# Optimization experiments

Measured on AMD Instinct MI355X. Metric: run time of the kernel, lower is better.

The kernel has to match this reference:

```python
import jax, jax.numpy as jnp
import numpy as np

DIM = 128
CODEBOOK_SIZE = 1024

def setup_inputs() -> dict:
    key = jax.random.key(0)
    k1, k2 = jax.random.split(key)
    x = jax.random.normal(k1, (16, 4096, DIM), dtype=jnp.float32)
    embed = jax.random.normal(k2, (CODEBOOK_SIZE, DIM), dtype=jnp.float32)
    return {"x": x, "embed": embed}

def reference(x, embed):
    # preprocess: flatten leading dims -> (N, d)
    shape = x.shape
    flat = x.reshape(-1, shape[-1])  # (N, d)
    x_sq = jnp.sum(flat * flat, axis=1, keepdims=True)        # (N, 1)
    e_sq = jnp.sum(embed * embed, axis=1)[None, :]            # (1, K)
    dist = -(x_sq - 2.0 * (flat @ embed.T) + e_sq)            # (N, K)
    embed_ind = jnp.argmax(dist, axis=-1)                     # (N,)
    embed_ind = embed_ind.reshape(shape[:-1])                 # (...,)
    quantize = jnp.take(embed, embed_ind, axis=0)             # (..., d)
    return (quantize, embed_ind)
```

## Files before the change

### kernel.cpp

```cpp
#include <hip/hip_runtime.h>

#define NRD   65536
#define DIMD  128
#define KCB   1024
#define RPB   64
#define NBLK  (NRD / RPB)
#define MARGIN 0.40f

typedef float f32x4 __attribute__((ext_vector_type(4)));
typedef short short8 __attribute__((ext_vector_type(8)));

#define WS_ESQ   0
#define WS_CNT   4096
#define WS_LIST  8192
#define WS_B     270336
#define WS_ET2   532480
#define WS_NEED  1056768

__device__ inline unsigned short f2bf(float f) {
    unsigned u = __float_as_uint(f);
    u += 0x7FFFu + ((u >> 16) & 1u);
    return (unsigned short)(u >> 16);
}

__device__ inline short8 pack_h(float4 a, float4 b) {
    short8 r;
    r[0]=(short)f2bf(a.x); r[1]=(short)f2bf(a.y); r[2]=(short)f2bf(a.z); r[3]=(short)f2bf(a.w);
    r[4]=(short)f2bf(b.x); r[5]=(short)f2bf(b.y); r[6]=(short)f2bf(b.z); r[7]=(short)f2bf(b.w);
    return r;
}

__global__ __launch_bounds__(256, 2) void prep_kernel(const float* __restrict__ embed,
                                                      float* __restrict__ esq,
                                                      float4* __restrict__ bblob,
                                                      float4* __restrict__ et4,
                                                      int* __restrict__ cnt,
                                                      int doTrans) {
    __shared__ float tile[64][129];
    const int t = threadIdx.x;
    {
        int gw   = blockIdx.x * 4 + (t >> 6);
        int lane = t & 63;
        const float* row = embed + (size_t)gw * DIMD;
        float a = row[lane], b = row[lane + 64];
        float v = a * a + b * b;
        #pragma unroll
        for (int off = 32; off >= 1; off >>= 1) v += __shfl_xor(v, off, 64);
        if (lane == 0) esq[gw] = v;
    }
    if (blockIdx.x < 64) {
        int tid  = blockIdx.x * 256 + t;
        int lane = tid & 63;
        int ctg  = (tid >> 6) & 15;
        int ksh  = (tid >> 10) & 1;
        int s    = tid >> 11;
        int chunk = s >> 1, kh = s & 1;
        int ks = kh * 2 + ksh;
        int l15 = lane & 15, l4 = lane >> 4;
        int code = chunk * 256 + ctg * 16 + l15;
        int d0   = ks * 32 + l4 * 8;
        const float4* e4 = (const float4*)(embed + (size_t)code * DIMD + d0);
        short8 v = pack_h(e4[0], e4[1]);
        bblob[tid] = *(float4*)&v;
    }
    if (doTrans && blockIdx.x >= 64 && blockIdx.x < 80) {
        const int c0 = (blockIdx.x - 64) * 64;
        #pragma unroll
        for (int i = 0; i < 8; ++i) {
            int u = t + i * 256;
            int row = u >> 5, col4 = u & 31;
            float4 v = ((const float4*)embed)[(size_t)(c0 + row) * 32 + col4];
            tile[row][col4 * 4 + 0] = v.x;
            tile[row][col4 * 4 + 1] = v.y;
            tile[row][col4 * 4 + 2] = v.z;
            tile[row][col4 * 4 + 3] = v.w;
        }
        __syncthreads();
        #pragma unroll
        for (int i = 0; i < 8; ++i) {
            int u = t + i * 256;
            int d = u >> 4, off = u & 15;
            float4 v;
            v.x = tile[off * 4 + 0][d];
            v.y = tile[off * 4 + 1][d];
            v.z = tile[off * 4 + 2][d];
            v.w = tile[off * 4 + 3][d];
            et4[(size_t)d * 256 + (c0 >> 2) + off] = v;
        }
    }
    if (blockIdx.x == 128 && t == 0) cnt[0] = 0;
}

__global__ __launch_bounds__(512, 4) void vq_mfma(const float* __restrict__ x,
                                                  const float* __restrict__ embed,
                                                  const float* __restrict__ esq,
                                                  const float4* __restrict__ bblob,
                                                  float* __restrict__ out_q,
                                                  float* __restrict__ out_idx,
                                                  int* __restrict__ cnt,
                                                  int* __restrict__ list) {
    __shared__ __align__(16) short Bb[32][512];
    __shared__ float rbest[4][RPB];
    __shared__ int   rmeta[4][RPB];
    __shared__ float rb2[4][RPB];

    const int t    = threadIdx.x;
    const int lane = t & 63;
    const int w    = __builtin_amdgcn_readfirstlane(t >> 6);
    const int rg   = w >> 2, cg = w & 3;
    const int l15  = lane & 15, l4 = lane >> 4;
    const int row0 = blockIdx.x * RPB;

    short (*Atrans)[4][512] = (short (*)[4][512])&Bb[0][0];

    const int ksA = w & 3, jh = w >> 2;
    const float4* xs = (const float4*)(x + (size_t)(row0 + lane) * DIMD + ksA * 32 + jh * 16);
    float4 xv0 = xs[0], xv1 = xs[1], xv2 = xs[2], xv3 = xs[3];

    const int rtA = lane >> 4, riA = lane & 15;
    *(short8*)&Atrans[ksA][rtA][((jh * 2 + 0) * 16 + riA) * 8] = pack_h(xv0, xv1);
    *(short8*)&Atrans[ksA][rtA][((jh * 2 + 1) * 16 + riA) * 8] = pack_h(xv2, xv3);
    asm volatile("s_waitcnt lgkmcnt(0)" ::: "memory");
    __builtin_amdgcn_s_barrier();

    short8 ahr[4][2];
    #pragma unroll
    for (int ks = 0; ks < 4; ++ks)
        #pragma unroll
        for (int rt = 0; rt < 2; ++rt)
            ahr[ks][rt] = *(const short8*)&Atrans[ks][rg * 2 + rt][lane * 8];
    asm volatile("s_waitcnt lgkmcnt(0)" ::: "memory");
    __builtin_amdgcn_s_barrier();

#define GLDS(sv) do {                                                                                   \
    const char* g_ = (const char*)bblob + (size_t)(sv) * 32768 + ((size_t)w * 64 + lane) * 16;          \
    _Pragma("unroll")                                                                                   \
    for (int k_ = 0; k_ < 4; ++k_)                                                                      \
        __builtin_amdgcn_global_load_lds(                                                               \
            (const __attribute__((address_space(1))) unsigned int*)(g_ + k_ * 8192),                    \
            (__attribute__((address_space(3))) unsigned int*)&Bb[k_ * 8 + w][0], 16, 0, 0);             \
} while (0)

    GLDS(0);
    asm volatile("s_waitcnt vmcnt(0)" ::: "memory");
    __builtin_amdgcn_s_barrier();

    f32x4 acc[2][4];
    float best[2][4]; int bidx[2][4]; float b2[2][4];
    #pragma unroll
    for (int i = 0; i < 2; ++i)
        #pragma unroll
        for (int j = 0; j < 4; ++j) { best[i][j] = -1e30f; bidx[i][j] = 0; b2[i][j] = -1e30f; }

    const float* esqp = esq + cg * 64 + l15;
    float eq0 = 0.f, eq1 = 0.f, eq2 = 0.f, eq3 = 0.f;

#define STEP(khv) do {                                                                  \
    const int s_ = c * 2 + khv;                                                         \
    if (khv == 0) {                                                                     \
        eq0 = esqp[c * 256];      eq1 = esqp[c * 256 + 16];                             \
        eq2 = esqp[c * 256 + 32]; eq3 = esqp[c * 256 + 48];                             \
        _Pragma("unroll")                                                               \
        for (int i_ = 0; i_ < 2; ++i_)                                                  \
            _Pragma("unroll")                                                           \
            for (int j_ = 0; j_ < 4; ++j_) acc[i_][j_] = (f32x4){0.f, 0.f, 0.f, 0.f};   \
    }                                                                                   \
    short8 bh_[2][4];                                                                   \
    _Pragma("unroll")                                                                   \
    for (int ksh_ = 0; ksh_ < 2; ++ksh_)                                                \
        _Pragma("unroll")                                                               \
        for (int ct_ = 0; ct_ < 4; ++ct_)                                               \
            bh_[ksh_][ct_] = *(const short8*)&Bb[ksh_ * 16 + cg * 4 + ct_][lane * 8];   \
    asm volatile("s_waitcnt lgkmcnt(0)" ::: "memory");                                  \
    __builtin_amdgcn_s_barrier();                            \
    if (s_ < 7) GLDS(s_ + 1);                                   \
    _Pragma("unroll")                                                                   \
    for (int ksh_ = 0; ksh_ < 2; ++ksh_) {                                              \
        _Pragma("unroll")                                                               \
        for (int ct_ = 0; ct_ < 4; ++ct_) {                                             \
            _Pragma("unroll")                                                           \
            for (int rt_ = 0; rt_ < 2; ++rt_)                                           \
                acc[rt_][ct_] = __builtin_amdgcn_mfma_f32_16x16x32_bf16(ahr[khv * 2 + ksh_][rt_], bh_[ksh_][ct_], acc[rt_][ct_], 0, 0, 0); \
        }                                                                               \
    }                                                                                   \
    if (khv == 1) {                           \
        _Pragma("unroll")                                                               \
        for (int ct_ = 0; ct_ < 4; ++ct_) {                                             \
            int code_ = c * 256 + cg * 64 + ct_ * 16 + l15;                             \
            float eq_ = (ct_ == 0) ? eq0 : (ct_ == 1) ? eq1 : (ct_ == 2) ? eq2 : eq3;   \
            _Pragma("unroll")                                                           \
            for (int rt_ = 0; rt_ < 2; ++rt_)                                           \
                _Pragma("unroll")                                                       \
                for (int r_ = 0; r_ < 4; ++r_) {                                        \
                    float sc_ = 2.0f * acc[rt_][ct_][r_] - eq_;                         \
                    b2[rt_][r_] = fmaxf(b2[rt_][r_], fminf(sc_, best[rt_][r_]));        \
                    if (sc_ > best[rt_][r_]) { best[rt_][r_] = sc_; bidx[rt_][r_] = code_; } \
                }                                                                       \
        }                                                                               \
    }                                                                                   \
    if (s_ < 7) {                                                                       \
        asm volatile("s_waitcnt vmcnt(0)" ::: "memory");          \
        __builtin_amdgcn_s_barrier();                                                   \
    }                                                                                   \
} while (0)

    for (int c = 0; c < 4; ++c) {
        STEP(0); STEP(1);
    }
#undef STEP
#undef GLDS

    #pragma unroll
    for (int rt = 0; rt < 2; ++rt)
        #pragma unroll
        for (int r = 0; r < 4; ++r) {
            float v = best[rt][r]; int i = bidx[rt][r]; float s2 = b2[rt][r];
            #pragma unroll
            for (int off = 1; off < 16; off <<= 1) {
                float ov = __shfl_xor(v, off, 64);
                int   oi = __shfl_xor(i, off, 64);
                float o2 = __shfl_xor(s2, off, 64);
                s2 = fmaxf(fmaxf(s2, o2), fminf(v, ov));
                bool sw = (ov > v) || (ov == v && oi < i);
                if (sw) { v = ov; i = oi; }
            }
            if (l15 == 0) {
                int rl = rg * 32 + rt * 16 + l4 * 4 + r;
                rbest[cg][rl] = v;
                rmeta[cg][rl] = i;
                rb2[cg][rl]   = s2;
            }
        }
    __syncthreads();
    if (t < RPB) {
        float b = rbest[0][t]; int i = rmeta[0][t]; float s2 = rb2[0][t];
        #pragma unroll
        for (int g = 1; g < 4; ++g) {
            float ob = rbest[g][t]; int oi = rmeta[g][t]; float o2 = rb2[g][t];
            s2 = fmaxf(fmaxf(s2, o2), fminf(b, ob));
            bool sw = (ob > b) || (ob == b && oi < i);
            if (sw) { b = ob; i = oi; }
        }
        out_idx[row0 + t] = (float)i;
        if (s2 >= b - MARGIN) { int pos = atomicAdd(cnt, 1); list[pos] = row0 + t; }
        rmeta[0][t] = i;
    }
    __syncthreads();
    {
        int row = t >> 3, part = t & 7;
        int idx = rmeta[0][row];
        const float4* src = (const float4*)(embed + (size_t)idx * DIMD + part * 16);
        float4* dst = (float4*)(out_q + (size_t)(row0 + row) * DIMD + part * 16);
        #pragma unroll
        for (int q = 0; q < 4; ++q) dst[q] = src[q];
    }
}

__global__ __launch_bounds__(256, 2) void trans_kernel(const float* __restrict__ embed,
                                                       float4* __restrict__ et4) {
    __shared__ float tile[64][129];
    const int t = threadIdx.x;
    const int c0 = blockIdx.x * 64;
    #pragma unroll
    for (int i = 0; i < 8; ++i) {
        int u = t + i * 256;
        int row = u >> 5, col4 = u & 31;
        float4 v = ((const float4*)embed)[(size_t)(c0 + row) * 32 + col4];
        tile[row][col4 * 4 + 0] = v.x;
        tile[row][col4 * 4 + 1] = v.y;
        tile[row][col4 * 4 + 2] = v.z;
        tile[row][col4 * 4 + 3] = v.w;
    }
    __syncthreads();
    #pragma unroll
    for (int i = 0; i < 8; ++i) {
        int u = t + i * 256;
        int d = u >> 4, off = u & 15;
        float4 v;
        v.x = tile[off * 4 + 0][d];
        v.y = tile[off * 4 + 1][d];
        v.z = tile[off * 4 + 2][d];
        v.w = tile[off * 4 + 3][d];
        et4[(size_t)d * 256 + (c0 >> 2) + off] = v;
    }
}

__global__ __launch_bounds__(256, 2) void refine_kernel(const float* __restrict__ x,
                                                        const float* __restrict__ embed,
                                                        const float* __restrict__ esq,
                                                        const f32x4* __restrict__ et4,
                                                        float* __restrict__ out_q,
                                                        float* __restrict__ out_idx,
                                                        const int* __restrict__ cnt,
                                                        const int* __restrict__ list) {
    __shared__ float xls[4][4][128];
    const int t = threadIdx.x, lane = t & 63, w = t >> 6;
    const int n = cnt[0];
    const int njobs = (n + 3) >> 2;
    for (int job = blockIdx.x * 4 + w; job < njobs; job += gridDim.x * 4) {
        int rows[4];
        #pragma unroll
        for (int i = 0; i < 4; ++i) {
            int li = job * 4 + i; if (li >= n) li = n - 1;
            rows[i] = list[li];
        }
        float xsq[4];
        #pragma unroll
        for (int i = 0; i < 4; ++i) {
            float2 xv = *(const float2*)(x + (size_t)rows[i] * DIMD + lane * 2);
            xls[w][i][lane * 2]     = xv.x;
            xls[w][i][lane * 2 + 1] = xv.y;
            float s = xv.x * xv.x + xv.y * xv.y;
            #pragma unroll
            for (int off = 32; off >= 1; off >>= 1) s += __shfl_xor(s, off, 64);
            xsq[i] = s;
        }
        f32x4 acc[4][4];
        #pragma unroll
        for (int i = 0; i < 4; ++i)
            #pragma unroll
            for (int g = 0; g < 4; ++g) acc[i][g] = (f32x4){0.f, 0.f, 0.f, 0.f};

        for (int d0 = 0; d0 < 32; ++d0) {
            float4 xd[4];
            #pragma unroll
            for (int i = 0; i < 4; ++i) xd[i] = *(const float4*)&xls[w][i][d0 * 4];
            #pragma unroll
            for (int dd = 0; dd < 4; ++dd) {
                const f32x4* ep = et4 + (size_t)(d0 * 4 + dd) * 256 + lane;
                f32x4 e0 = ep[0], e1 = ep[64], e2 = ep[128], e3 = ep[192];
                #pragma unroll
                for (int i = 0; i < 4; ++i) {
                    float xsc = (dd == 0) ? xd[i].x : (dd == 1) ? xd[i].y
                              : (dd == 2) ? xd[i].z : xd[i].w;
                    acc[i][0] = e0 * xsc + acc[i][0];
                    acc[i][1] = e1 * xsc + acc[i][1];
                    acc[i][2] = e2 * xsc + acc[i][2];
                    acc[i][3] = e3 * xsc + acc[i][3];
                }
            }
        }

        #pragma unroll
        for (int i = 0; i < 4; ++i) {
            float bv = -1e30f; int bi = 0;
            #pragma unroll
            for (int g = 0; g < 4; ++g) {
                float4 eq = *(const float4*)&esq[g * 256 + lane * 4];
                #pragma unroll
                for (int c2 = 0; c2 < 4; ++c2) {
                    float eqv = (c2 == 0) ? eq.x : (c2 == 1) ? eq.y : (c2 == 2) ? eq.z : eq.w;
                    float sc = -(__fadd_rn(__fsub_rn(xsq[i], __fmul_rn(2.0f, acc[i][g][c2])), eqv));
                    int code = g * 256 + lane * 4 + c2;
                    if (sc > bv) { bv = sc; bi = code; }
                }
            }
            #pragma unroll
            for (int off = 32; off >= 1; off >>= 1) {
                float ov = __shfl_xor(bv, off, 64);
                int   oi = __shfl_xor(bi, off, 64);
                if (ov > bv || (ov == bv && oi < bi)) { bv = ov; bi = oi; }
            }
            if (lane == 0) out_idx[rows[i]] = (float)bi;
            if (lane < 32) {
                float4 v = ((const float4*)embed)[(size_t)bi * 32 + lane];
                ((float4*)out_q)[(size_t)rows[i] * 32 + lane] = v;
            }
        }
    }
}

extern "C" void kernel_launch(void* const* d_in, const int* in_sizes, int n_in,
                              void* d_out, int out_size, void* d_ws, size_t ws_size,
                              hipStream_t stream) {
    const float* x     = (const float*)d_in[0];
    const float* embed = (const float*)d_in[1];
    float* out     = (float*)d_out;
    float* out_q   = out;
    float* out_idx = out + (size_t)NRD * DIMD;

    char*  wsb  = (char*)d_ws;
    float* esq  = (float*)(wsb + WS_ESQ);
    int*   cnt  = (int*)(wsb + WS_CNT);
    int*   list = (int*)(wsb + WS_LIST);
    float4* bblob = (float4*)(wsb + WS_B);

    const int fused = (ws_size >= (size_t)WS_NEED) ? 1 : 0;
    f32x4* et4 = fused ? (f32x4*)(wsb + WS_ET2) : (f32x4*)(wsb + WS_B);

    prep_kernel  <<<dim3(256),  dim3(256), 0, stream>>>(embed, esq, bblob, (float4*)et4, cnt, fused);
    vq_mfma      <<<dim3(NBLK), dim3(512), 0, stream>>>(x, embed, esq, bblob, out_q, out_idx, cnt, list);
    if (!fused)
        trans_kernel<<<dim3(16), dim3(256), 0, stream>>>(embed, (float4*)et4);
    refine_kernel<<<dim3(512),  dim3(256), 0, stream>>>(x, embed, esq, et4, out_q, out_idx, cnt, list);
}
```

Baseline: 80.80 us.

## Double-buffer codebook LDS tiles and stage e_sq in shared memory

```diff
diff --git a/kernel.cpp b/kernel.cpp
--- a/kernel.cpp
+++ b/kernel.cpp
@@ -99,7 +99,8 @@
                                                   float* __restrict__ out_idx,
                                                   int* __restrict__ cnt,
                                                   int* __restrict__ list) {
-    __shared__ __align__(16) short Bb[32][512];
+    __shared__ __align__(16) short Bb[2][32][512];
+    __shared__ float esqs[KCB];
     __shared__ float rbest[4][RPB];
     __shared__ int   rmeta[4][RPB];
     __shared__ float rb2[4][RPB];
@@ -111,39 +112,42 @@
     const int l15  = lane & 15, l4 = lane >> 4;
     const int row0 = blockIdx.x * RPB;
 
-    short (*Atrans)[4][512] = (short (*)[4][512])&Bb[0][0];
+    short (*Atrans)[4][512] = (short (*)[4][512])&Bb[1][0][0];
+
+    const float2 ev = *(const float2*)(esq + t * 2);
 
     const int ksA = w & 3, jh = w >> 2;
     const float4* xs = (const float4*)(x + (size_t)(row0 + lane) * DIMD + ksA * 32 + jh * 16);
     float4 xv0 = xs[0], xv1 = xs[1], xv2 = xs[2], xv3 = xs[3];
 
-    const int rtA = lane >> 4, riA = lane & 15;
-    *(short8*)&Atrans[ksA][rtA][((jh * 2 + 0) * 16 + riA) * 8] = pack_h(xv0, xv1);
-    *(short8*)&Atrans[ksA][rtA][((jh * 2 + 1) * 16 + riA) * 8] = pack_h(xv2, xv3);
-    asm volatile("s_waitcnt lgkmcnt(0)" ::: "memory");
-    __builtin_amdgcn_s_barrier();
-
-    short8 ahr[4][2];
-    #pragma unroll
-    for (int ks = 0; ks < 4; ++ks)
-        #pragma unroll
-        for (int rt = 0; rt < 2; ++rt)
-            ahr[ks][rt] = *(const short8*)&Atrans[ks][rg * 2 + rt][lane * 8];
-    asm volatile("s_waitcnt lgkmcnt(0)" ::: "memory");
-    __builtin_amdgcn_s_barrier();
-
-#define GLDS(sv) do {                                                                                   \
+#define GLDS(sv, bufv) do {                                                                             \
     const char* g_ = (const char*)bblob + (size_t)(sv) * 32768 + ((size_t)w * 64 + lane) * 16;          \
     _Pragma("unroll")                                                                                   \
     for (int k_ = 0; k_ < 4; ++k_)                                                                      \
         __builtin_amdgcn_global_load_lds(                                                               \
             (const __attribute__((address_space(1))) unsigned int*)(g_ + k_ * 8192),                    \
-            (__attribute__((address_space(3))) unsigned int*)&Bb[k_ * 8 + w][0], 16, 0, 0);             \
+            (__attribute__((address_space(3))) unsigned int*)&Bb[bufv][k_ * 8 + w][0], 16, 0, 0);       \
 } while (0)
 
-    GLDS(0);
-    asm volatile("s_waitcnt vmcnt(0)" ::: "memory");
+    GLDS(0, 0);
+
+    const int rtA = lane >> 4, riA = lane & 15;
+    *(short8*)&Atrans[ksA][rtA][((jh * 2 + 0) * 16 + riA) * 8] = pack_h(xv0, xv1);
+    *(short8*)&Atrans[ksA][rtA][((jh * 2 + 1) * 16 + riA) * 8] = pack_h(xv2, xv3);
+    *(float2*)&esqs[t * 2] = ev;
+    asm volatile("s_waitcnt lgkmcnt(0)" ::: "memory");
     __builtin_amdgcn_s_barrier();
+
+    short8 ahr[4][2];
+    #pragma unroll
+    for (int ks = 0; ks < 4; ++ks)
+        #pragma unroll
+        for (int rt = 0; rt < 2; ++rt)
+            ahr[ks][rt] = *(const short8*)&Atrans[ks][rg * 2 + rt][lane * 8];
+    asm volatile("s_waitcnt lgkmcnt(0)" ::: "memory");
+    __builtin_amdgcn_s_barrier();
+
+    GLDS(1, 1);
 
     f32x4 acc[2][4];
     float best[2][4]; int bidx[2][4]; float b2[2][4];
@@ -152,38 +156,41 @@
         #pragma unroll
         for (int j = 0; j < 4; ++j) { best[i][j] = -1e30f; bidx[i][j] = 0; b2[i][j] = -1e30f; }
 
-    const float* esqp = esq + cg * 64 + l15;
     float eq0 = 0.f, eq1 = 0.f, eq2 = 0.f, eq3 = 0.f;
 
 #define STEP(khv) do {                                                                  \
-    const int s_ = c * 2 + khv;                                                         \
-    if (khv == 0) {                                                                     \
-        eq0 = esqp[c * 256];      eq1 = esqp[c * 256 + 16];                             \
-        eq2 = esqp[c * 256 + 32]; eq3 = esqp[c * 256 + 48];                             \
+    if ((khv) == 1 && c == 3) { asm volatile("s_waitcnt vmcnt(0)" ::: "memory"); }      \
+    else                      { asm volatile("s_waitcnt vmcnt(4)" ::: "memory"); }      \
+    __builtin_amdgcn_s_barrier();                   \
+    short8 bh_[2][4];                                                                   \
+    _Pragma("unroll")                                                                   \
+    for (int ksh_ = 0; ksh_ < 2; ++ksh_)                                                \
+        _Pragma("unroll")                                                               \
+        for (int ct_ = 0; ct_ < 4; ++ct_)                                               \
+            bh_[ksh_][ct_] = *(const short8*)&Bb[khv][ksh_ * 16 + cg * 4 + ct_][lane * 8]; \
+    if ((khv) == 0) {                                                                   \
+        eq0 = esqs[c * 256 + cg * 64 + l15];                                            \
+        eq1 = esqs[c * 256 + cg * 64 + l15 + 16];                                       \
+        eq2 = esqs[c * 256 + cg * 64 + l15 + 32];                                       \
+        eq3 = esqs[c * 256 + cg * 64 + l15 + 48];                                       \
         _Pragma("unroll")                                                               \
         for (int i_ = 0; i_ < 2; ++i_)                                                  \
             _Pragma("unroll")                                                           \
             for (int j_ = 0; j_ < 4; ++j_) acc[i_][j_] = (f32x4){0.f, 0.f, 0.f, 0.f};   \
     }                                                                                   \
-    short8 bh_[2][4];                                                                   \
-    _Pragma("unroll")                                                                   \
-    for (int ksh_ = 0; ksh_ < 2; ++ksh_)                                                \
-        _Pragma("unroll")                                                               \
-        for (int ct_ = 0; ct_ < 4; ++ct_)                                               \
-            bh_[ksh_][ct_] = *(const short8*)&Bb[ksh_ * 16 + cg * 4 + ct_][lane * 8];   \
     asm volatile("s_waitcnt lgkmcnt(0)" ::: "memory");                                  \
-    __builtin_amdgcn_s_barrier();                            \
-    if (s_ < 7) GLDS(s_ + 1);                                   \
+    __builtin_amdgcn_s_barrier();                        \
+    if (c < 3) GLDS(c * 2 + 2 + (khv), (khv));        \
     _Pragma("unroll")                                                                   \
     for (int ksh_ = 0; ksh_ < 2; ++ksh_) {                                              \
         _Pragma("unroll")                                                               \
         for (int ct_ = 0; ct_ < 4; ++ct_) {                                             \
             _Pragma("unroll")                                                           \
             for (int rt_ = 0; rt_ < 2; ++rt_)                                           \
-                acc[rt_][ct_] = __builtin_amdgcn_mfma_f32_16x16x32_bf16(ahr[khv * 2 + ksh_][rt_], bh_[ksh_][ct_], acc[rt_][ct_], 0, 0, 0); \
+                acc[rt_][ct_] = __builtin_amdgcn_mfma_f32_16x16x32_bf16(ahr[(khv) * 2 + ksh_][rt_], bh_[ksh_][ct_], acc[rt_][ct_], 0, 0, 0); \
         }                                                                               \
     }                                                                                   \
-    if (khv == 1) {                           \
+    if ((khv) == 1) {                         \
         _Pragma("unroll")                                                               \
         for (int ct_ = 0; ct_ < 4; ++ct_) {                                             \
             int code_ = c * 256 + cg * 64 + ct_ * 16 + l15;                             \
@@ -198,10 +205,6 @@
                 }                                                                       \
         }                                                                               \
     }                                                                                   \
-    if (s_ < 7) {                                                                       \
-        asm volatile("s_waitcnt vmcnt(0)" ::: "memory");          \
-        __builtin_amdgcn_s_barrier();                                                   \
-    }                                                                                   \
 } while (0)
 
     for (int c = 0; c < 4; ++c) {
```

Result: slower. 144.8 us (+79.2%).
